# Kernel optimization log

Hardware: AMD Instinct MI355X
Metric: run time of the kernel (lower is better)

Reference implementation:

```python
import jax, jax.numpy as jnp
import numpy as np

NUM_SUB = 2  # top-k experts kept by the gate


def setup_inputs() -> dict:
    key = jax.random.key(0)
    kx, kr, kw = jax.random.split(key, 3)
    B, C, H, W, E = 16, 256, 64, 64, 8
    inputs = jax.random.normal(kx, (B, C, H, W), dtype=jnp.float32)
    W_router = jax.random.normal(kr, (C, E), dtype=jnp.float32) / np.sqrt(C)
    b_router = jnp.zeros((E,), dtype=jnp.float32)
    W_exp = jax.random.normal(kw, (E, C, C), dtype=jnp.float32) / np.sqrt(C)
    b_exp = jnp.zeros((E, C), dtype=jnp.float32)
    return {"inputs": inputs, "W_router": W_router, "b_router": b_router,
            "W_exp": W_exp, "b_exp": b_exp, "k": 2}


def reference(inputs, W_router, b_router, W_exp, b_exp, k):
    # Router: global-avg-pool + linear -> [B, E]
    E = W_router.shape[1]
    pooled = inputs.mean(axis=(2, 3))                       # [B, C]
    logits = pooled @ W_router + b_router                   # [B, E]
    # softmax in fp32 then cast back (matches F.softmax(..., dtype=torch.float))
    weights = jax.nn.softmax(logits.astype(jnp.float32), axis=1).astype(inputs.dtype)
    # top-k gating: scatter of gathered values == weights * topk-mask
    _, topk_idx = jax.lax.top_k(weights, NUM_SUB)            # [B, k]
    mask = jax.nn.one_hot(topk_idx, E, dtype=weights.dtype).sum(axis=1)  # [B, E]
    exp_w = weights * mask                                   # sparse gates [B, E]
    # out = inputs + sum_e gate[b,e] * (conv1x1_e(inputs))
    # expert weight W_exp[e, d, c]: out_d = sum_c W[d,c] x_c + b_d
    out = inputs \
        + jnp.einsum('be,edc,bchw->bdhw', exp_w, W_exp, inputs) \
        + jnp.einsum('be,ed->bd', exp_w, b_exp)[:, :, None, None]
    return out
```

## Files before the change

### kernel.cpp

```cpp
#include <hip/hip_runtime.h>
#include <hip/hip_bf16.h>

typedef __bf16 bf16x8 __attribute__((ext_vector_type(8)));
typedef float f32x4 __attribute__((ext_vector_type(4)));
typedef unsigned short ushort4v __attribute__((ext_vector_type(4)));
typedef unsigned short ushort8v __attribute__((ext_vector_type(8)));

#define B_  16
#define C_  256
#define HW_ 4096
#define E_  8

__device__ inline unsigned short f2bf(float f) {
    unsigned int b = __builtin_bit_cast(unsigned int, f);
    b += 0x7FFFu + ((b >> 16) & 1u);
    return (unsigned short)(b >> 16);
}

__global__ __launch_bounds__(256) void k_pool(const float* __restrict__ in,
                                              float* __restrict__ pooled) {
    int bc = blockIdx.x;
    const float* p = in + (size_t)bc * HW_;
    int t = threadIdx.x;
    float s = 0.f;
#pragma unroll
    for (int i = 0; i < 4; i++) {
        float4 v = *reinterpret_cast<const float4*>(p + (size_t)(t + i * 256) * 4);
        s += v.x + v.y + v.z + v.w;
    }
#pragma unroll
    for (int off = 32; off; off >>= 1) s += __shfl_down(s, off, 64);
    __shared__ float part[4];
    if ((t & 63) == 0) part[t >> 6] = s;
    __syncthreads();
    if (t == 0) pooled[bc] = (part[0] + part[1] + part[2] + part[3]) * (1.0f / HW_);
}

__global__ __launch_bounds__(256) void k_router3(const float* __restrict__ pooled,
                                                 const float* __restrict__ Wr,
                                                 const float* __restrict__ br,
                                                 const float* __restrict__ bexp,
                                                 float* __restrict__ gates,
                                                 float* __restrict__ biasE) {
    __shared__ float pl[B_ * C_];
    __shared__ float wrs[C_ * E_];
    __shared__ float lgh[B_ * E_][2];
    __shared__ float gs[B_][E_];
    int t = threadIdx.x;
#pragma unroll
    for (int i = 0; i < 4; ++i)
        reinterpret_cast<float4*>(pl)[t + i * 256] =
            reinterpret_cast<const float4*>(pooled)[t + i * 256];
#pragma unroll
    for (int i = 0; i < 2; ++i)
        reinterpret_cast<float4*>(wrs)[t + i * 256] =
            reinterpret_cast<const float4*>(Wr)[t + i * 256];
    __syncthreads();
    {
        int pair = t >> 1, half = t & 1;
        int b = pair >> 3, e = pair & 7;
        float s = 0.f;
        int c0 = half * 128;
        for (int c = c0; c < c0 + 128; ++c) s += pl[b * C_ + c] * wrs[c * E_ + e];
        lgh[pair][half] = s;
    }
    __syncthreads();
    if (t < B_) {
        float w[E_];
        float m = -1e30f;
#pragma unroll
        for (int e = 0; e < E_; ++e) {
            w[e] = lgh[t * E_ + e][0] + lgh[t * E_ + e][1] + br[e];
            m = fmaxf(m, w[e]);
        }
        float sum = 0.f;
#pragma unroll
        for (int e = 0; e < E_; ++e) { w[e] = __expf(w[e] - m); sum += w[e]; }
        float inv = 1.f / sum;
#pragma unroll
        for (int e = 0; e < E_; ++e) w[e] *= inv;
        int i0 = 0;
#pragma unroll
        for (int e = 1; e < E_; ++e) if (w[e] > w[i0]) i0 = e;
        int i1 = -1;
#pragma unroll
        for (int e = 0; e < E_; ++e) {
            if (e == i0) continue;
            if (i1 < 0 || w[e] > w[i1]) i1 = e;
        }
#pragma unroll
        for (int e = 0; e < E_; ++e) {
            float g = (e == i0 || e == i1) ? w[e] : 0.f;
            gs[t][e] = g;
            gates[t * E_ + e] = g;
        }
    }
    __syncthreads();
    {
        int d = t;
        float acc[B_];
#pragma unroll
        for (int b = 0; b < B_; ++b) acc[b] = 0.f;
#pragma unroll
        for (int e = 0; e < E_; ++e) {
            float w = bexp[e * C_ + d];
#pragma unroll
            for (int b = 0; b < B_; ++b) acc[b] += gs[b][e] * w;
        }
#pragma unroll
        for (int b = 0; b < B_; ++b) biasE[b * C_ + d] = acc[b];
    }
}

__global__ __launch_bounds__(256) void k_weff(const float* __restrict__ Wexp,
                                              const float* __restrict__ gates,
                                              unsigned short* __restrict__ Weff) {
    int b = blockIdx.y;
    int dblk = blockIdx.x;
    __shared__ float g[E_];
    int t = threadIdx.x;
    if (t < E_) g[t] = gates[b * E_ + t];
    __syncthreads();
    int dloc = t >> 5, cq = t & 31;
    int d = dblk * 8 + dloc;
#pragma unroll
    for (int half = 0; half < 2; half++) {
        int c = (cq + half * 32) * 4;
        float4 acc = {0.f, 0.f, 0.f, 0.f};
#pragma unroll
        for (int e = 0; e < E_; e++) {
            float ge = g[e];
            if (ge != 0.f) {
                float4 w = *reinterpret_cast<const float4*>(
                    Wexp + ((size_t)(e * C_ + d)) * C_ + c);
                acc.x += ge * w.x; acc.y += ge * w.y;
                acc.z += ge * w.z; acc.w += ge * w.w;
            }
        }
        ushort4v o = { f2bf(acc.x), f2bf(acc.y), f2bf(acc.z), f2bf(acc.w) };
        *reinterpret_cast<ushort4v*>(Weff + ((size_t)(b * C_ + d)) * C_ + c) = o;
    }
}

#define TSLD 68

__global__ __launch_bounds__(512, 4) void k_fused(const float* __restrict__ in,
                                                  const unsigned short* __restrict__ Weff,
                                                  const float* __restrict__ biasE,
                                                  float* __restrict__ out) {
    __shared__ unsigned short Bs[64 * 256];
    __shared__ float Ts[64 * TSLD];
    const int t = threadIdx.x;
    const int b = blockIdx.y;
    const int n0 = blockIdx.x * 64;
    const int lane = t & 63, w = t >> 6;
    const int kg = lane >> 4, lr = lane & 15;
    const float* inB = in + (size_t)b * C_ * HW_ + n0;
    const unsigned short* Wb = Weff + (size_t)b * C_ * C_;
    const unsigned short* aptr = Wb + (size_t)(w * 32 + lr) * C_ + kg * 8;

    bf16x8 a0[2], a1[2];
#pragma unroll
    for (int mi = 0; mi < 2; ++mi)
        a0[mi] = __builtin_bit_cast(bf16x8,
            *reinterpret_cast<const ushort8v*>(aptr + mi * 16 * C_));

    {
        const int cl = t >> 3;
        const int pq = (t & 7) * 8;
        const int pr = t & 63;
        const int cq = t >> 6;
        for (int pass = 0; pass < 4; ++pass) {
            const float* src = inB + (size_t)(pass * 64 + cl) * HW_ + pq;
            float4 v0 = *reinterpret_cast<const float4*>(src);
            float4 v1 = *reinterpret_cast<const float4*>(src + 4);
            *reinterpret_cast<float4*>(&Ts[cl * TSLD + pq]) = v0;
            *reinterpret_cast<float4*>(&Ts[cl * TSLD + pq + 4]) = v1;
            __syncthreads();
            ushort8v u;
#pragma unroll
            for (int j = 0; j < 8; ++j)
                u[j] = f2bf(Ts[(cq * 8 + j) * TSLD + pr]);
            const int chunk = (pass * 8 + cq) ^ (pr & 7);
            *reinterpret_cast<ushort8v*>(&Bs[pr * 256 + chunk * 8]) = u;
            __syncthreads();
        }
    }

    f32x4 acc[2][4];
#pragma unroll
    for (int mi = 0; mi < 2; ++mi) {
#pragma unroll
        for (int j = 0; j < 4; ++j) {
            const int row = w * 32 + mi * 16 + kg * 4 + j;
            const float bias = biasE[b * C_ + row];
#pragma unroll
            for (int ni = 0; ni < 4; ++ni) {
                const int p = ni * 16 + lr;
                unsigned short xv =
                    Bs[p * 256 + (((row >> 3) ^ (p & 7)) * 8) + (row & 7)];
                float xf = __builtin_bit_cast(float, (unsigned int)xv << 16);
                acc[mi][ni][j] = xf + bias;
            }
        }
    }

#pragma unroll
    for (int kf = 0; kf < 8; kf += 2) {
#pragma unroll
        for (int mi = 0; mi < 2; ++mi)
            a1[mi] = __builtin_bit_cast(bf16x8,
                *reinterpret_cast<const ushort8v*>(aptr + mi * 16 * C_ + (kf + 1) * 32));
        {
            bf16x8 bfv[4];
#pragma unroll
            for (int ni = 0; ni < 4; ++ni) {
                const int p = ni * 16 + lr;
                bfv[ni] = __builtin_bit_cast(bf16x8,
                    *reinterpret_cast<const ushort8v*>(
                        &Bs[p * 256 + (((kf * 4 + kg) ^ (lr & 7)) * 8)]));
            }
#pragma unroll
            for (int mi = 0; mi < 2; ++mi)
#pragma unroll
                for (int ni = 0; ni < 4; ++ni)
                    acc[mi][ni] = __builtin_amdgcn_mfma_f32_16x16x32_bf16(
                        a0[mi], bfv[ni], acc[mi][ni], 0, 0, 0);
        }
        if (kf + 2 < 8) {
#pragma unroll
            for (int mi = 0; mi < 2; ++mi)
                a0[mi] = __builtin_bit_cast(bf16x8,
                    *reinterpret_cast<const ushort8v*>(aptr + mi * 16 * C_ + (kf + 2) * 32));
        }
        {
            bf16x8 bfv[4];
#pragma unroll
            for (int ni = 0; ni < 4; ++ni) {
                const int p = ni * 16 + lr;
                bfv[ni] = __builtin_bit_cast(bf16x8,
                    *reinterpret_cast<const ushort8v*>(
                        &Bs[p * 256 + ((((kf + 1) * 4 + kg) ^ (lr & 7)) * 8)]));
            }
#pragma unroll
            for (int mi = 0; mi < 2; ++mi)
#pragma unroll
                for (int ni = 0; ni < 4; ++ni)
                    acc[mi][ni] = __builtin_amdgcn_mfma_f32_16x16x32_bf16(
                        a1[mi], bfv[ni], acc[mi][ni], 0, 0, 0);
        }
    }

    float* outB = out + (size_t)b * C_ * HW_ + n0;
#pragma unroll
    for (int mi = 0; mi < 2; ++mi) {
#pragma unroll
        for (int j = 0; j < 4; ++j) {
            const int row = w * 32 + mi * 16 + kg * 4 + j;
            float* orow = outB + (size_t)row * HW_;
#pragma unroll
            for (int ni = 0; ni < 4; ++ni)
                orow[ni * 16 + lr] = acc[mi][ni][j];
        }
    }
}

extern "C" void kernel_launch(void* const* d_in, const int* in_sizes, int n_in,
                              void* d_out, int out_size, void* d_ws, size_t ws_size,
                              hipStream_t stream) {
    const float* in   = (const float*)d_in[0];
    const float* Wr   = (const float*)d_in[1];
    const float* br   = (const float*)d_in[2];
    const float* Wexp = (const float*)d_in[3];
    const float* bexp = (const float*)d_in[4];
    float* out = (float*)d_out;
    char* ws = (char*)d_ws;

    float* pooled         = (float*)(ws);
    float* gates          = (float*)(ws + 0x10000);
    float* biasE          = (float*)(ws + 0x11000);
    unsigned short* Weff  = (unsigned short*)(ws + 0x20000);

    hipLaunchKernelGGL(k_pool,    dim3(B_ * C_), dim3(256), 0, stream, in, pooled);
    hipLaunchKernelGGL(k_router3, dim3(1),       dim3(256), 0, stream,
                       pooled, Wr, br, bexp, gates, biasE);
    hipLaunchKernelGGL(k_weff,    dim3(32, B_),  dim3(256), 0, stream, Wexp, gates, Weff);
    hipLaunchKernelGGL(k_fused,   dim3(HW_ / 64, B_), dim3(512), 0, stream,
                       in, Weff, biasE, out);
}
```

Before: 55.24 us.

## Halve fused block to 256 threads with 64-row warp tiles and bf16 transpose staging

The fused GEMM block drops from 512 to 256 threads, and each wave now computes 64 output rows instead of 32. The input transpose converts to bf16 before staging, using a smaller padded u32 tile, and the per-block bias is cached in shared memory. The explicit double-buffered prefetch of A fragments from global memory is removed in favour of a simple per-k-step load. The intent is less LDS traffic and footprint plus more MFMA work per wave, in exchange for more registers per thread and more serial passes in the transpose.

```diff
diff --git a/kernel.cpp b/kernel.cpp
--- a/kernel.cpp
+++ b/kernel.cpp
@@ -142,121 +142,101 @@
     }
 }
 
-#define TSLD 68
-
-__global__ __launch_bounds__(512, 4) void k_fused(const float* __restrict__ in,
+__global__ __launch_bounds__(256, 4) void k_fused(const float* __restrict__ in,
                                                   const unsigned short* __restrict__ Weff,
                                                   const float* __restrict__ biasE,
                                                   float* __restrict__ out) {
     __shared__ unsigned short Bs[64 * 256];
-    __shared__ float Ts[64 * TSLD];
-    const int t = threadIdx.x;
-    const int b = blockIdx.y;
+    __shared__ unsigned int   TsU[32 * 33];
+    __shared__ float biasS[256];
+
+    const int t  = threadIdx.x;
+    const int b  = blockIdx.y;
     const int n0 = blockIdx.x * 64;
     const int lane = t & 63, w = t >> 6;
     const int kg = lane >> 4, lr = lane & 15;
-    const float* inB = in + (size_t)b * C_ * HW_ + n0;
-    const unsigned short* Wb = Weff + (size_t)b * C_ * C_;
-    const unsigned short* aptr = Wb + (size_t)(w * 32 + lr) * C_ + kg * 8;
-
-    bf16x8 a0[2], a1[2];
-#pragma unroll
-    for (int mi = 0; mi < 2; ++mi)
-        a0[mi] = __builtin_bit_cast(bf16x8,
-            *reinterpret_cast<const ushort8v*>(aptr + mi * 16 * C_));
+    const float* Xb = in + ((size_t)b * C_) * HW_ + n0;
+    const unsigned short* Ab = Weff + (size_t)b * C_ * C_;
+
+    biasS[t] = biasE[b * C_ + t];
 
     {
         const int cl = t >> 3;
         const int pq = (t & 7) * 8;
         const int pr = t & 63;
-        const int cq = t >> 6;
-        for (int pass = 0; pass < 4; ++pass) {
-            const float* src = inB + (size_t)(pass * 64 + cl) * HW_ + pq;
+        const int c4 = t >> 6;
+        for (int pass = 0; pass < 8; ++pass) {
+            const float* src = Xb + (size_t)(pass * 32 + cl) * HW_ + pq;
             float4 v0 = *reinterpret_cast<const float4*>(src);
             float4 v1 = *reinterpret_cast<const float4*>(src + 4);
-            *reinterpret_cast<float4*>(&Ts[cl * TSLD + pq]) = v0;
-            *reinterpret_cast<float4*>(&Ts[cl * TSLD + pq + 4]) = v1;
+            unsigned int* tr = &TsU[cl * 33 + (t & 7) * 4];
+            tr[0] = (unsigned int)f2bf(v0.x) | ((unsigned int)f2bf(v0.y) << 16);
+            tr[1] = (unsigned int)f2bf(v0.z) | ((unsigned int)f2bf(v0.w) << 16);
+            tr[2] = (unsigned int)f2bf(v1.x) | ((unsigned int)f2bf(v1.y) << 16);
+            tr[3] = (unsigned int)f2bf(v1.z) | ((unsigned int)f2bf(v1.w) << 16);
             __syncthreads();
             ushort8v u;
-#pragma unroll
-            for (int j = 0; j < 8; ++j)
-                u[j] = f2bf(Ts[(cq * 8 + j) * TSLD + pr]);
-            const int chunk = (pass * 8 + cq) ^ (pr & 7);
-            *reinterpret_cast<ushort8v*>(&Bs[pr * 256 + chunk * 8]) = u;
+            const int half = pr & 1;
+#pragma unroll
+            for (int j = 0; j < 8; ++j) {
+                unsigned int wv = TsU[(c4 * 8 + j) * 33 + (pr >> 1)];
+                u[j] = (unsigned short)(half ? (wv >> 16) : (wv & 0xffff));
+            }
+            const int cs = (pass * 4 + c4) ^ (pr & 7);
+            *reinterpret_cast<ushort8v*>(&Bs[pr * 256 + cs * 8]) = u;
             __syncthreads();
         }
     }
 
-    f32x4 acc[2][4];
-#pragma unroll
-    for (int mi = 0; mi < 2; ++mi) {
+    f32x4 acc[4][4];
+#pragma unroll
+    for (int mi = 0; mi < 4; ++mi) {
 #pragma unroll
         for (int j = 0; j < 4; ++j) {
-            const int row = w * 32 + mi * 16 + kg * 4 + j;
-            const float bias = biasE[b * C_ + row];
+            const int row = w * 64 + mi * 16 + kg * 4 + j;
+            const float bias = biasS[row];
 #pragma unroll
             for (int ni = 0; ni < 4; ++ni) {
                 const int p = ni * 16 + lr;
                 unsigned short xv =
                     Bs[p * 256 + (((row >> 3) ^ (p & 7)) * 8) + (row & 7)];
-                float xf = __builtin_bit_cast(float, (unsigned int)xv << 16);
-                acc[mi][ni][j] = xf + bias;
+                acc[mi][ni][j] =
+                    __builtin_bit_cast(float, (unsigned int)xv << 16) + bias;
             }
         }
     }
 
 #pragma unroll
-    for (int kf = 0; kf < 8; kf += 2) {
-#pragma unroll
-        for (int mi = 0; mi < 2; ++mi)
-            a1[mi] = __builtin_bit_cast(bf16x8,
-                *reinterpret_cast<const ushort8v*>(aptr + mi * 16 * C_ + (kf + 1) * 32));
-        {
-            bf16x8 bfv[4];
-#pragma unroll
-            for (int ni = 0; ni < 4; ++ni) {
-                const int p = ni * 16 + lr;
-                bfv[ni] = __builtin_bit_cast(bf16x8,
-                    *reinterpret_cast<const ushort8v*>(
-                        &Bs[p * 256 + (((kf * 4 + kg) ^ (lr & 7)) * 8)]));
-            }
-#pragma unroll
-            for (int mi = 0; mi < 2; ++mi)
-#pragma unroll
-                for (int ni = 0; ni < 4; ++ni)
-                    acc[mi][ni] = __builtin_amdgcn_mfma_f32_16x16x32_bf16(
-                        a0[mi], bfv[ni], acc[mi][ni], 0, 0, 0);
-        }
-        if (kf + 2 < 8) {
-#pragma unroll
-            for (int mi = 0; mi < 2; ++mi)
-                a0[mi] = __builtin_bit_cast(bf16x8,
-                    *reinterpret_cast<const ushort8v*>(aptr + mi * 16 * C_ + (kf + 2) * 32));
-        }
-        {
-            bf16x8 bfv[4];
-#pragma unroll
-            for (int ni = 0; ni < 4; ++ni) {
-                const int p = ni * 16 + lr;
-                bfv[ni] = __builtin_bit_cast(bf16x8,
-                    *reinterpret_cast<const ushort8v*>(
-                        &Bs[p * 256 + ((((kf + 1) * 4 + kg) ^ (lr & 7)) * 8)]));
-            }
-#pragma unroll
-            for (int mi = 0; mi < 2; ++mi)
-#pragma unroll
-                for (int ni = 0; ni < 4; ++ni)
-                    acc[mi][ni] = __builtin_amdgcn_mfma_f32_16x16x32_bf16(
-                        a1[mi], bfv[ni], acc[mi][ni], 0, 0, 0);
-        }
-    }
-
-    float* outB = out + (size_t)b * C_ * HW_ + n0;
-#pragma unroll
-    for (int mi = 0; mi < 2; ++mi) {
+    for (int kf = 0; kf < 8; ++kf) {
+        bf16x8 afr[4], bfv[4];
+#pragma unroll
+        for (int mi = 0; mi < 4; ++mi) {
+            const int row = w * 64 + mi * 16 + lr;
+            afr[mi] = __builtin_bit_cast(bf16x8,
+                *reinterpret_cast<const ushort8v*>(
+                    &Ab[(size_t)row * C_ + kf * 32 + kg * 8]));
+        }
+#pragma unroll
+        for (int ni = 0; ni < 4; ++ni) {
+            const int p = ni * 16 + lr;
+            const int cc = (kf * 4 + kg) ^ (p & 7);
+            bfv[ni] = __builtin_bit_cast(bf16x8,
+                *reinterpret_cast<const ushort8v*>(&Bs[p * 256 + cc * 8]));
+        }
+#pragma unroll
+        for (int mi = 0; mi < 4; ++mi)
+#pragma unroll
+            for (int ni = 0; ni < 4; ++ni)
+                acc[mi][ni] = __builtin_amdgcn_mfma_f32_16x16x32_bf16(
+                    afr[mi], bfv[ni], acc[mi][ni], 0, 0, 0);
+    }
+
+    float* outB = out + ((size_t)b * C_) * HW_ + n0;
+#pragma unroll
+    for (int mi = 0; mi < 4; ++mi) {
 #pragma unroll
         for (int j = 0; j < 4; ++j) {
-            const int row = w * 32 + mi * 16 + kg * 4 + j;
+            const int row = w * 64 + mi * 16 + kg * 4 + j;
             float* orow = outB + (size_t)row * HW_;
 #pragma unroll
             for (int ni = 0; ni < 4; ++ni)
@@ -285,6 +265,6 @@
     hipLaunchKernelGGL(k_router3, dim3(1),       dim3(256), 0, stream,
                        pooled, Wr, br, bexp, gates, biasE);
     hipLaunchKernelGGL(k_weff,    dim3(32, B_),  dim3(256), 0, stream, Wexp, gates, Weff);
-    hipLaunchKernelGGL(k_fused,   dim3(HW_ / 64, B_), dim3(512), 0, stream,
+    hipLaunchKernelGGL(k_fused,   dim3(HW_ / 64, B_), dim3(256), 0, stream,
                        in, Weff, biasE, out);
 }
```

Measured after the change: 59.60 us. 1.08x slower.
